# Optimization experiments

Measured on AMD Instinct MI355X. Metric: run time of the kernel, lower is better.

## Reference

```python
import jax, jax.numpy as jnp
import numpy as np

B, S, D, H, FF = 4, 2048, 512, 8, 2048
HD = D // H
SCALE = float(D) ** 0.5  # original scales by sqrt(embed_dim), not sqrt(head_dim)
EPS = 1e-5


def setup_inputs() -> dict:
    key = jax.random.key(0)
    ks = jax.random.split(key, 16)
    s_in = 1.0 / np.sqrt(D)
    s_ff = 1.0 / np.sqrt(FF)
    return {
        "embeddings": jax.random.normal(ks[0], (B, S, D), dtype=jnp.float32),
        "mask": jnp.ones((B, S), dtype=bool),
        # per-head Q/K/V projections stacked: [H, D, HD]
        "Wq": jax.random.uniform(ks[1], (H, D, HD), jnp.float32, -s_in, s_in),
        "bq": jax.random.uniform(ks[2], (H, HD), jnp.float32, -s_in, s_in),
        "Wk": jax.random.uniform(ks[3], (H, D, HD), jnp.float32, -s_in, s_in),
        "bk": jax.random.uniform(ks[4], (H, HD), jnp.float32, -s_in, s_in),
        "Wv": jax.random.uniform(ks[5], (H, D, HD), jnp.float32, -s_in, s_in),
        "bv": jax.random.uniform(ks[6], (H, HD), jnp.float32, -s_in, s_in),
        "Wc": jax.random.uniform(ks[7], (D, D), jnp.float32, -s_in, s_in),
        "bc": jax.random.uniform(ks[8], (D,), jnp.float32, -s_in, s_in),
        "W1": jax.random.uniform(ks[9], (D, FF), jnp.float32, -s_in, s_in),
        "b1": jax.random.uniform(ks[10], (FF,), jnp.float32, -s_in, s_in),
        "W2": jax.random.uniform(ks[11], (FF, D), jnp.float32, -s_ff, s_ff),
        "b2": jax.random.uniform(ks[12], (D,), jnp.float32, -s_ff, s_ff),
        "gamma": jnp.ones((D,), jnp.float32),
        "beta": jnp.zeros((D,), jnp.float32),
    }


def reference(embeddings, mask, Wq, bq, Wk, bk, Wv, bv, Wc, bc, W1, b1, W2, b2, gamma, beta):
    # Per-head projections batched into one einsum each: [B,H,S,HD]
    Q = jnp.einsum("bsd,hdf->bhsf", embeddings, Wq) + bq[:, None, :]
    K = jnp.einsum("bsd,hdf->bhsf", embeddings, Wk) + bk[:, None, :]
    V = jnp.einsum("bsd,hdf->bhsf", embeddings, Wv) + bv[:, None, :]
    # NOTE: the original computes a masked score tensor but then softmaxes the
    # UNMASKED scores (bug). We faithfully ignore the mask here.
    scores = jnp.einsum("bhsf,bhtf->bhst", Q, K) / SCALE  # [B,H,S,S]
    A = jax.nn.softmax(scores, axis=-1)
    Hh = jnp.einsum("bhst,bhtf->bhsf", A, V)  # [B,H,S,HD]
    # concat heads along feature dim (head h -> contiguous slice)
    Hcat = jnp.transpose(Hh, (0, 2, 1, 3)).reshape(B, S, D)
    Hp = Hcat @ Wc + bc
    # add & norm (dropout is identity at eval)
    res = Hp + embeddings
    mu = jnp.mean(res, axis=-1, keepdims=True)
    var = jnp.var(res, axis=-1, keepdims=True)
    Hn = (res - mu) / jnp.sqrt(var + EPS) * gamma + beta
    out = jax.nn.relu(Hn @ W1 + b1) @ W2 + b2  # no residual after FFN in original
    return out, mask
```

## Files before the change

### kernel.cpp

```cpp
#include <hip/hip_runtime.h>
#include <hip/hip_bf16.h>
#include <cstdint>
#include <cstddef>

typedef short  s16x8 __attribute__((ext_vector_type(8)));
typedef short  s16x4 __attribute__((ext_vector_type(4)));
typedef float  f32x4 __attribute__((ext_vector_type(4)));
typedef unsigned u32x2 __attribute__((ext_vector_type(2)));

static constexpr int Bb = 4, Ss = 2048, Dd = 512, Hh = 8, HDd = 64, FFf = 2048;
static constexpr int Mm = Bb * Ss;

__device__ __forceinline__ unsigned short f2bf(float f) {
  unsigned u = __float_as_uint(f);
  u += 0x7FFFu + ((u >> 16) & 1u);
  return (unsigned short)(u >> 16);
}

__device__ __forceinline__ unsigned cvt_pk_bf16(float lo, float hi) {
  unsigned r;
  asm("v_cvt_pk_bf16_f32 %0, %1, %2" : "=v"(r) : "v"(lo), "v"(hi));
  return r;
}

__device__ __forceinline__ float exp2_raw(float x) {
  float r;
  asm("v_exp_f32 %0, %1\n\ts_nop 0" : "=v"(r) : "v"(x));
  return r;
}

#define GLOAD_LDS16(gp, lp)                                                     \
  __builtin_amdgcn_global_load_lds((const __attribute__((address_space(1))) void*)(gp), \
                                   (__attribute__((address_space(3))) void*)(lp), 16, 0, 0)

__device__ __forceinline__ void xpose_tile(const float* __restrict__ in,
                                           unsigned short* __restrict__ out,
                                           int K, int N, int bx, int by, float (*t)[33]) {
  const int lx = threadIdx.x & 31, ly = threadIdx.x >> 5;
  const int n0 = bx * 32, k0 = by * 32;
#pragma unroll
  for (int r = 0; r < 4; ++r) t[ly + r * 8][lx] = in[(size_t)(k0 + ly + r * 8) * N + n0 + lx];
  __syncthreads();
#pragma unroll
  for (int r = 0; r < 4; ++r)
    out[(size_t)(n0 + ly + r * 8) * K + k0 + lx] = f2bf(t[lx][ly + r * 8]);
}

__global__ __launch_bounds__(256) void prep_all(
    const float* __restrict__ emb, const float* __restrict__ Wq, const float* __restrict__ Wk,
    const float* __restrict__ Wv, const float* __restrict__ Wc, const float* __restrict__ W1,
    const float* __restrict__ W2, unsigned short* __restrict__ embB,
    unsigned short* __restrict__ WtQKV, unsigned short* __restrict__ WtC,
    unsigned short* __restrict__ Wt1, unsigned short* __restrict__ Wt2,
    float* __restrict__ maskOut) {
  __shared__ float t[32][33];
  const int blk = blockIdx.x;
  if (blk < 4096) {
    const int i = blk * 256 + threadIdx.x;
    const float4 v = reinterpret_cast<const float4*>(emb)[i];
    s16x4 o; o[0] = f2bf(v.x); o[1] = f2bf(v.y); o[2] = f2bf(v.z); o[3] = f2bf(v.w);
    reinterpret_cast<s16x4*>(embB)[i] = o;
  } else if (blk < 4864) {
    const int b = blk - 4096;
    const int bx = b & 15, by = (b >> 4) & 1, z = b >> 5;
    const int sel = z >> 3, h = z & 7;
    const float* W = sel == 0 ? Wq : (sel == 1 ? Wk : Wv);
    const float* inb = W + (size_t)h * 512 * 64;
    unsigned short* outb = WtQKV + (size_t)sel * 512 * 512 + (size_t)h * 64 * 512;
    const int lx = threadIdx.x & 31, ly = threadIdx.x >> 5;
    const int d0 = bx * 32, f0 = by * 32;
#pragma unroll
    for (int r = 0; r < 4; ++r) t[ly + r * 8][lx] = inb[(size_t)(d0 + ly + r * 8) * 64 + f0 + lx];
    __syncthreads();
#pragma unroll
    for (int r = 0; r < 4; ++r)
      outb[(size_t)(f0 + ly + r * 8) * 512 + d0 + lx] = f2bf(t[lx][ly + r * 8]);
  } else if (blk < 5120) {
    const int b = blk - 4864;
    xpose_tile(Wc, WtC, 512, 512, b & 15, b >> 4, t);
  } else if (blk < 6144) {
    const int b = blk - 5120;
    xpose_tile(W1, Wt1, 512, 2048, b & 63, b >> 6, t);
  } else if (blk < 7168) {
    const int b = blk - 6144;
    xpose_tile(W2, Wt2, 2048, 512, b & 15, b >> 4, t);
  } else {
    const int i = (blk - 7168) * 256 + threadIdx.x;
    if (i < Bb * Ss) maskOut[i] = 1.0f;
  }
}

__global__ __launch_bounds__(256) void vtrans(const unsigned short* __restrict__ Vn,
                                              unsigned short* __restrict__ Vt) {
  __shared__ unsigned short t[64][72];
  const int bh = blockIdx.y, s0 = blockIdx.x * 64;
  const int row = threadIdx.x >> 2, cs = (threadIdx.x & 3) << 4;
  const unsigned short* src = Vn + (((size_t)bh * 2048 + s0 + row) << 6) + cs;
  *reinterpret_cast<s16x8*>(&t[row][cs]) = *reinterpret_cast<const s16x8*>(src);
  *reinterpret_cast<s16x8*>(&t[row][cs + 8]) = *reinterpret_cast<const s16x8*>(src + 8);
  __syncthreads();
  unsigned ow[8];
#pragma unroll
  for (int j = 0; j < 8; ++j)
    ow[j] = (unsigned)t[cs + 2 * j][row] | ((unsigned)t[cs + 2 * j + 1][row] << 16);
  unsigned short* dst = Vt + (((size_t)bh * 64 + row) << 11) + s0 + cs;
  *reinterpret_cast<uint4*>(dst) = *reinterpret_cast<const uint4*>(&ow[0]);
  *reinterpret_cast<uint4*>(dst + 8) = *reinterpret_cast<const uint4*>(&ow[4]);
}

template<int EPI, int NI>
__global__ __launch_bounds__(256) void gemm_bt(
    const unsigned short* __restrict__ A, const unsigned short* __restrict__ Bt,
    const float* __restrict__ bias0, const float* __restrict__ bias1, const float* __restrict__ bias2,
    const float* __restrict__ addf, float* __restrict__ outF,
    unsigned short* __restrict__ outB0, unsigned short* __restrict__ outB1,
    unsigned short* __restrict__ outB2, int M, int N, int K, int nbx) {
  constexpr int BN = NI * 32;
  __shared__ alignas(16) unsigned short As[3][128 * 32];
  __shared__ alignas(16) unsigned short Bs[3][BN * 32];
  const int tid = threadIdx.x;
  const int lane = tid & 63, wid = tid >> 6;
  const int wr = wid >> 1, wc = wid & 1;
  const int fr = lane & 15, kg = lane >> 4;

  const int lin = blockIdx.x;
  const int xcd = lin & 7, idx = lin >> 3;
  const int bx = idx % nbx, ysub = idx / nbx;
  const int m0 = (xcd * 8 + ysub) * 128, n0 = bx * BN;

  const int srow = tid >> 2;
  const int schunk = (tid & 3) ^ ((tid >> 3) & 3);
  const unsigned short* gA = A + (size_t)(m0 + srow) * K + (schunk << 3);
  const unsigned short* gB = Bt + (size_t)(n0 + srow) * K + (schunk << 3);

  auto STAGE = [&](int kt, int buf) {
    unsigned short* lA = &As[buf][wid * 512];
    unsigned short* lB = &Bs[buf][wid * 512];
    GLOAD_LDS16(gA + kt, lA);
    GLOAD_LDS16(gA + (size_t)64 * K + kt, lA + 2048);
    GLOAD_LDS16(gB + kt, lB);
    if constexpr (NI == 4) GLOAD_LDS16(gB + (size_t)64 * K + kt, lB + 2048);
  };

  f32x4 acc[4][NI];
#pragma unroll
  for (int i = 0; i < 4; ++i)
#pragma unroll
    for (int j = 0; j < NI; ++j)
#pragma unroll
      for (int r = 0; r < 4; ++r) acc[i][j][r] = 0.f;

  STAGE(0, 0);
  STAGE(32, 1);
  const int nk = K >> 5;
  int cur = 0;
  const int rchunk = (kg ^ ((fr >> 1) & 3)) << 3;
  for (int ki = 0; ki < nk; ++ki) {
    const int pre = cur == 0 ? 2 : cur - 1;
    __builtin_amdgcn_s_barrier();
    if (ki + 2 < nk) {
      STAGE((ki + 2) << 5, pre);
      if constexpr (NI == 4)
        asm volatile("s_waitcnt vmcnt(8)" ::: "memory");
      else
        asm volatile("s_waitcnt vmcnt(6)" ::: "memory");
    } else if (ki + 1 < nk) {
      if constexpr (NI == 4)
        asm volatile("s_waitcnt vmcnt(4)" ::: "memory");
      else
        asm volatile("s_waitcnt vmcnt(3)" ::: "memory");
    } else {
      asm volatile("s_waitcnt vmcnt(0)" ::: "memory");
    }
    __builtin_amdgcn_sched_barrier(0);
    __builtin_amdgcn_s_barrier();
    __builtin_amdgcn_sched_barrier(0);

    s16x8 af[4], bfv[NI];
#pragma unroll
    for (int i = 0; i < 4; ++i)
      af[i] = *reinterpret_cast<const s16x8*>(&As[cur][(wr * 64 + i * 16 + fr) * 32 + rchunk]);
#pragma unroll
    for (int i = 0; i < NI; ++i)
      bfv[i] = *reinterpret_cast<const s16x8*>(
          &Bs[cur][(wc * (NI * 16) + i * 16 + fr) * 32 + rchunk]);
    __builtin_amdgcn_s_setprio(1);
#pragma unroll
    for (int mi = 0; mi < 4; ++mi)
#pragma unroll
      for (int ni = 0; ni < NI; ++ni)
        acc[mi][ni] = __builtin_amdgcn_mfma_f32_16x16x32_bf16(af[mi], bfv[ni], acc[mi][ni], 0, 0, 0);
    __builtin_amdgcn_s_setprio(0);
    cur = cur == 2 ? 0 : cur + 1;
  }

#pragma unroll
  for (int mi = 0; mi < 4; ++mi)
#pragma unroll
    for (int ni = 0; ni < NI; ++ni)
#pragma unroll
      for (int r = 0; r < 4; ++r) {
        const int row = m0 + wr * 64 + mi * 16 + kg * 4 + r;
        const int col = n0 + wc * (NI * 16) + ni * 16 + fr;
        float v = acc[mi][ni][r];
        if constexpr (EPI == 0) {
          const int sel = col >> 9, c = col & 511;
          const float* bs = sel == 0 ? bias0 : (sel == 1 ? bias1 : bias2);
          v += bs[c];
          const int b = row >> 11, s = row & 2047;
          const int h = c >> 6, f = c & 63;
          unsigned short* ob = sel == 0 ? outB0 : (sel == 1 ? outB1 : outB2);
          ob[((size_t)((b << 3) + h) * 2048 + s) * 64 + f] = f2bf(v);
        } else if constexpr (EPI == 1) {
          const size_t idx2 = (size_t)row * 512 + col;
          outF[idx2] = v + bias0[col] + addf[idx2];
        } else if constexpr (EPI == 2) {
          v += bias0[col];
          outB0[(size_t)row * 2048 + col] = f2bf(v > 0.f ? v : 0.f);
        } else {
          outF[(size_t)row * 512 + col] = v + bias0[col];
        }
      }
}

__global__ __launch_bounds__(256) void attn_kernel(const unsigned short* __restrict__ Q,
                                                   const unsigned short* __restrict__ Kx,
                                                   const unsigned short* __restrict__ V,
                                                   unsigned short* __restrict__ Hcat) {
  const int lane = threadIdx.x & 63, wid = threadIdx.x >> 6;
  const int fr = lane & 15, kg = lane >> 4;
  const int lin = blockIdx.x;
  const int xcd = lin & 7, idx = lin >> 3;
  const int bh = xcd * 4 + (idx & 3);
  const int qi = idx >> 2;
  const int b = bh >> 3, h = bh & 7;
  const int q0 = qi * 64 + wid * 16;
  const unsigned short* Qh = Q + (size_t)bh * Ss * HDd;
  const unsigned short* Kh = Kx + (size_t)bh * Ss * HDd;
  const unsigned short* Vh = V + (size_t)bh * HDd * Ss;

  __shared__ alignas(16) unsigned short Ks[2][64 * 64];
  __shared__ alignas(16) unsigned short Vs[64 * 64];
  __shared__ alignas(16) unsigned short P[4][16][72];

  const int srow = lane >> 3;
  const int scol = ((lane & 7) ^ srow) << 3;
  const unsigned short* gK0 = Kh + (size_t)(8 * (2 * wid + 0) + srow) * 64 + scol;
  const unsigned short* gK1 = Kh + (size_t)(8 * (2 * wid + 1) + srow) * 64 + scol;
  const unsigned short* gV0 = Vh + (size_t)(8 * (2 * wid + 0) + srow) * 2048 + scol;
  const unsigned short* gV1 = Vh + (size_t)(8 * (2 * wid + 1) + srow) * 2048 + scol;
  unsigned short* lK0a = &Ks[0][(2 * wid + 0) * 512];
  unsigned short* lK1a = &Ks[0][(2 * wid + 1) * 512];
  unsigned short* lK0b = &Ks[1][(2 * wid + 0) * 512];
  unsigned short* lK1b = &Ks[1][(2 * wid + 1) * 512];
  unsigned short* lV0 = &Vs[(2 * wid + 0) * 512];
  unsigned short* lV1 = &Vs[(2 * wid + 1) * 512];

  s16x8 bq[2];
#pragma unroll
  for (int kb = 0; kb < 2; ++kb)
    bq[kb] = *reinterpret_cast<const s16x8*>(&Qh[(size_t)(q0 + fr) * 64 + kb * 32 + kg * 8]);

  f32x4 o[4];
#pragma unroll
  for (int ct = 0; ct < 4; ++ct)
#pragma unroll
    for (int r = 0; r < 4; ++r) o[ct][r] = 0.f;
  float mr = -1e30f, lsum = 0.f;

  const float iscL = 1.4426950408889634f * 0.044194173824159216f;
  const int swz = (fr & 7) << 3;

  GLOAD_LDS16(gK0, lK0a);
  GLOAD_LDS16(gK1, lK1a);
  GLOAD_LDS16(gV0, lV0);
  GLOAD_LDS16(gV1, lV1);

#pragma unroll 1
  for (int t = 0; t < 32; ++t) {
    const int kt = t * 64;
    const int ktn = (kt + 64) & 2047;
    const unsigned short* KsC = Ks[t & 1];
    unsigned short* nK0 = (t & 1) ? lK0a : lK0b;
    unsigned short* nK1 = (t & 1) ? lK1a : lK1b;

    asm volatile("s_waitcnt vmcnt(2)" ::: "memory");
    __builtin_amdgcn_sched_barrier(0);
    __builtin_amdgcn_s_barrier();
    __builtin_amdgcn_sched_barrier(0);

    f32x4 sc[4];
#pragma unroll
    for (int ct = 0; ct < 4; ++ct)
#pragma unroll
      for (int r = 0; r < 4; ++r) sc[ct][r] = 0.f;
    __builtin_amdgcn_s_setprio(1);
#pragma unroll
    for (int ct = 0; ct < 4; ++ct)
#pragma unroll
      for (int kb = 0; kb < 2; ++kb) {
        const s16x8 kf = *reinterpret_cast<const s16x8*>(
            &KsC[(ct * 16 + fr) * 64 + (((kg << 3) + (kb << 5)) ^ swz)]);
        sc[ct] = __builtin_amdgcn_mfma_f32_16x16x32_bf16(kf, bq[kb], sc[ct], 0, 0, 0);
      }
    __builtin_amdgcn_s_setprio(0);

    GLOAD_LDS16(gK0 + (size_t)ktn * 64, nK0);
    GLOAD_LDS16(gK1 + (size_t)ktn * 64, nK1);

    float mxl;
    {
      const float a0 = fmaxf(fmaxf(sc[0][0], sc[0][1]), fmaxf(sc[0][2], sc[0][3]));
      const float a1 = fmaxf(fmaxf(sc[1][0], sc[1][1]), fmaxf(sc[1][2], sc[1][3]));
      const float a2 = fmaxf(fmaxf(sc[2][0], sc[2][1]), fmaxf(sc[2][2], sc[2][3]));
      const float a3 = fmaxf(fmaxf(sc[3][0], sc[3][1]), fmaxf(sc[3][2], sc[3][3]));
      mxl = fmaxf(fmaxf(a0, a1), fmaxf(a2, a3)) * iscL;
    }
    if (!__all(mxl <= mr + 8.0f)) {
      float mx = fmaxf(mxl, __shfl_xor(mxl, 16));
      mx = fmaxf(mx, __shfl_xor(mx, 32));
      const float mn = fmaxf(mr, mx);
      const float corr = exp2_raw(mr - mn);
      mr = mn;
      lsum *= corr;
      float corrq[4];
#pragma unroll
      for (int r = 0; r < 4; ++r) corrq[r] = __shfl(corr, kg * 4 + r);
#pragma unroll
      for (int ct = 0; ct < 4; ++ct)
#pragma unroll
        for (int r = 0; r < 4; ++r) o[ct][r] *= corrq[r];
    }

    float ps0 = 0.f, ps1 = 0.f;
#pragma unroll
    for (int ct = 0; ct < 4; ++ct) {
      float p0 = exp2_raw(__builtin_fmaf(sc[ct][0], iscL, -mr));
      float p1 = exp2_raw(__builtin_fmaf(sc[ct][1], iscL, -mr));
      float p2 = exp2_raw(__builtin_fmaf(sc[ct][2], iscL, -mr));
      float p3 = exp2_raw(__builtin_fmaf(sc[ct][3], iscL, -mr));
      ps0 += (p0 + p1);
      ps1 += (p2 + p3);
      u32x2 pk;
      pk[0] = cvt_pk_bf16(p0, p1);
      pk[1] = cvt_pk_bf16(p2, p3);
      *reinterpret_cast<u32x2*>(&P[wid][fr][ct * 16 + kg * 4]) = pk;
    }
    lsum += ps0 + ps1;

    asm volatile("s_waitcnt vmcnt(2)" ::: "memory");
    __builtin_amdgcn_sched_barrier(0);
    __builtin_amdgcn_s_barrier();
    __builtin_amdgcn_sched_barrier(0);

    const s16x8 pa0 = *reinterpret_cast<const s16x8*>(&P[wid][fr][kg * 8]);
    const s16x8 pa1 = *reinterpret_cast<const s16x8*>(&P[wid][fr][32 + kg * 8]);
    __builtin_amdgcn_s_setprio(1);
#pragma unroll
    for (int ct = 0; ct < 4; ++ct) {
      const s16x8 bv0 = *reinterpret_cast<const s16x8*>(
          &Vs[(ct * 16 + fr) * 64 + (((kg << 3) + 0) ^ swz)]);
      o[ct] = __builtin_amdgcn_mfma_f32_16x16x32_bf16(pa0, bv0, o[ct], 0, 0, 0);
      const s16x8 bv1 = *reinterpret_cast<const s16x8*>(
          &Vs[(ct * 16 + fr) * 64 + (((kg << 3) + 32) ^ swz)]);
      o[ct] = __builtin_amdgcn_mfma_f32_16x16x32_bf16(pa1, bv1, o[ct], 0, 0, 0);
    }
    __builtin_amdgcn_s_setprio(0);

    __builtin_amdgcn_s_barrier();
    __builtin_amdgcn_sched_barrier(0);
    GLOAD_LDS16(gV0 + ktn, lV0);
    GLOAD_LDS16(gV1 + ktn, lV1);
  }

  lsum += __shfl_xor(lsum, 16);
  lsum += __shfl_xor(lsum, 32);
  float invq[4];
#pragma unroll
  for (int r = 0; r < 4; ++r) invq[r] = 1.0f / __shfl(lsum, kg * 4 + r);
#pragma unroll
  for (int ct = 0; ct < 4; ++ct)
#pragma unroll
    for (int r = 0; r < 4; ++r) {
      const int qrow = q0 + kg * 4 + r;
      Hcat[(size_t)(b * Ss + qrow) * Dd + h * 64 + ct * 16 + fr] = f2bf(o[ct][r] * invq[r]);
    }
}

__global__ __launch_bounds__(256) void layernorm_k(const float* __restrict__ res,
                                                   const float* __restrict__ gamma,
                                                   const float* __restrict__ beta,
                                                   unsigned short* __restrict__ out) {
  const int lane = threadIdx.x & 63, wid = threadIdx.x >> 6;
  const int row = blockIdx.x * 4 + wid;
  const float* rp = res + (size_t)row * 512 + lane * 8;
  const float4 v0 = *reinterpret_cast<const float4*>(rp);
  const float4 v1 = *reinterpret_cast<const float4*>(rp + 4);
  float x[8] = {v0.x, v0.y, v0.z, v0.w, v1.x, v1.y, v1.z, v1.w};
  float s = 0.f, q = 0.f;
#pragma unroll
  for (int j = 0; j < 8; ++j) { s += x[j]; q += x[j] * x[j]; }
#pragma unroll
  for (int off = 32; off; off >>= 1) { s += __shfl_xor(s, off); q += __shfl_xor(q, off); }
  const float mean = s * (1.f / 512.f);
  const float var = q * (1.f / 512.f) - mean * mean;
  const float rstd = rsqrtf(var + 1e-5f);
  s16x8 o;
#pragma unroll
  for (int j = 0; j < 8; ++j) {
    const int c = lane * 8 + j;
    o[j] = f2bf((x[j] - mean) * rstd * gamma[c] + beta[c]);
  }
  *reinterpret_cast<s16x8*>(out + (size_t)row * 512 + lane * 8) = o;
}

extern "C" void kernel_launch(void* const* d_in, const int* in_sizes, int n_in,
                              void* d_out, int out_size, void* d_ws, size_t ws_size,
                              hipStream_t stream) {
  const float* emb = (const float*)d_in[0];
  const float* Wq = (const float*)d_in[2];
  const float* bq = (const float*)d_in[3];
  const float* Wk = (const float*)d_in[4];
  const float* bk = (const float*)d_in[5];
  const float* Wv = (const float*)d_in[6];
  const float* bv = (const float*)d_in[7];
  const float* Wc = (const float*)d_in[8];
  const float* bc = (const float*)d_in[9];
  const float* W1 = (const float*)d_in[10];
  const float* b1 = (const float*)d_in[11];
  const float* W2 = (const float*)d_in[12];
  const float* b2 = (const float*)d_in[13];
  const float* gamma = (const float*)d_in[14];
  const float* beta = (const float*)d_in[15];
  float* out = (float*)d_out;

  char* ws = (char*)d_ws;
  size_t off = 0;
  auto alloc = [&](size_t bytes) {
    char* p = ws + off;
    off = (off + bytes + 255) & ~(size_t)255;
    return p;
  };
  unsigned short* embB = (unsigned short*)alloc((size_t)Mm * Dd * 2);
  unsigned short* WtQKV = (unsigned short*)alloc((size_t)1536 * 512 * 2);
  unsigned short* WtC = (unsigned short*)alloc((size_t)512 * 512 * 2);
  unsigned short* Wt1 = (unsigned short*)alloc((size_t)2048 * 512 * 2);
  unsigned short* Wt2 = (unsigned short*)alloc((size_t)512 * 2048 * 2);
  unsigned short* Qb = (unsigned short*)alloc((size_t)Mm * Dd * 2);
  unsigned short* Kb = (unsigned short*)alloc((size_t)Mm * Dd * 2);
  unsigned short* Vt = (unsigned short*)alloc((size_t)Mm * Dd * 2);
  unsigned short* Hcat = (unsigned short*)alloc((size_t)Mm * Dd * 2);
  float* resF = (float*)alloc((size_t)Mm * Dd * 4);
  unsigned short* HnB = (unsigned short*)alloc((size_t)Mm * Dd * 2);
  unsigned short* G = Qb;
  unsigned short* Vn = HnB;

  prep_all<<<7200, 256, 0, stream>>>(emb, Wq, Wk, Wv, Wc, W1, W2,
                                     embB, WtQKV, WtC, Wt1, Wt2,
                                     out + (size_t)Mm * Dd);

  gemm_bt<0, 4><<<768, 256, 0, stream>>>(embB, WtQKV, bq, bk, bv, nullptr, nullptr,
                                         Qb, Kb, Vn, Mm, 1536, 512, 12);
  vtrans<<<dim3(32, 32), 256, 0, stream>>>(Vn, Vt);
  attn_kernel<<<1024, 256, 0, stream>>>(Qb, Kb, Vt, Hcat);
  gemm_bt<1, 2><<<512, 256, 0, stream>>>(Hcat, WtC, bc, nullptr, nullptr, emb, resF,
                                         nullptr, nullptr, nullptr, Mm, 512, 512, 8);
  layernorm_k<<<2048, 256, 0, stream>>>(resF, gamma, beta, HnB);
  gemm_bt<2, 4><<<1024, 256, 0, stream>>>(HnB, Wt1, b1, nullptr, nullptr, nullptr, nullptr,
                                          G, nullptr, nullptr, Mm, 2048, 512, 16);
  gemm_bt<3, 2><<<512, 256, 0, stream>>>(G, Wt2, b2, nullptr, nullptr, nullptr, out,
                                         nullptr, nullptr, nullptr, Mm, 512, 2048, 8);
}
```

Measured before the change: 177.5 us.

## Fuse V transpose into QKV GEMM epilogue and double attention block size

The QKV projection epilogue now writes V directly in transposed [bh, f, s] layout using packed 4-element stores, which removes the separate vtrans kernel launch and its extra read and write of V. The attention kernel moves to 512-thread blocks covering 128 query rows. Each wave now issues one K and one V tile load instead of two, and half as many blocks each reuse a K/V tile across twice as many queries. The larger blocks may lower occupancy and add barrier cost across eight waves.

```diff
diff --git a/kernel.cpp b/kernel.cpp
--- a/kernel.cpp
+++ b/kernel.cpp
@@ -90,24 +90,6 @@
   }
 }
 
-__global__ __launch_bounds__(256) void vtrans(const unsigned short* __restrict__ Vn,
-                                              unsigned short* __restrict__ Vt) {
-  __shared__ unsigned short t[64][72];
-  const int bh = blockIdx.y, s0 = blockIdx.x * 64;
-  const int row = threadIdx.x >> 2, cs = (threadIdx.x & 3) << 4;
-  const unsigned short* src = Vn + (((size_t)bh * 2048 + s0 + row) << 6) + cs;
-  *reinterpret_cast<s16x8*>(&t[row][cs]) = *reinterpret_cast<const s16x8*>(src);
-  *reinterpret_cast<s16x8*>(&t[row][cs + 8]) = *reinterpret_cast<const s16x8*>(src + 8);
-  __syncthreads();
-  unsigned ow[8];
-#pragma unroll
-  for (int j = 0; j < 8; ++j)
-    ow[j] = (unsigned)t[cs + 2 * j][row] | ((unsigned)t[cs + 2 * j + 1][row] << 16);
-  unsigned short* dst = Vt + (((size_t)bh * 64 + row) << 11) + s0 + cs;
-  *reinterpret_cast<uint4*>(dst) = *reinterpret_cast<const uint4*>(&ow[0]);
-  *reinterpret_cast<uint4*>(dst + 8) = *reinterpret_cast<const uint4*>(&ow[4]);
-}
-
 template<int EPI, int NI>
 __global__ __launch_bounds__(256) void gemm_bt(
     const unsigned short* __restrict__ A, const unsigned short* __restrict__ Bt,
@@ -197,33 +179,52 @@
 #pragma unroll
   for (int mi = 0; mi < 4; ++mi)
 #pragma unroll
-    for (int ni = 0; ni < NI; ++ni)
-#pragma unroll
-      for (int r = 0; r < 4; ++r) {
-        const int row = m0 + wr * 64 + mi * 16 + kg * 4 + r;
+    for (int ni = 0; ni < NI; ++ni) {
+      if constexpr (EPI == 0) {
         const int col = n0 + wc * (NI * 16) + ni * 16 + fr;
-        float v = acc[mi][ni][r];
-        if constexpr (EPI == 0) {
-          const int sel = col >> 9, c = col & 511;
-          const float* bs = sel == 0 ? bias0 : (sel == 1 ? bias1 : bias2);
-          v += bs[c];
-          const int b = row >> 11, s = row & 2047;
-          const int h = c >> 6, f = c & 63;
-          unsigned short* ob = sel == 0 ? outB0 : (sel == 1 ? outB1 : outB2);
-          ob[((size_t)((b << 3) + h) * 2048 + s) * 64 + f] = f2bf(v);
-        } else if constexpr (EPI == 1) {
-          const size_t idx2 = (size_t)row * 512 + col;
-          outF[idx2] = v + bias0[col] + addf[idx2];
-        } else if constexpr (EPI == 2) {
-          v += bias0[col];
-          outB0[(size_t)row * 2048 + col] = f2bf(v > 0.f ? v : 0.f);
+        const int sel = col >> 9, c = col & 511;
+        const int h = c >> 6, f = c & 63;
+        const int row0 = m0 + wr * 64 + mi * 16 + kg * 4;
+        const int b = row0 >> 11, s0 = row0 & 2047;
+        if (sel == 2) {
+          const float bsv = bias2[c];
+          u32x2 pk;
+          pk[0] = (unsigned)f2bf(acc[mi][ni][0] + bsv) |
+                  ((unsigned)f2bf(acc[mi][ni][1] + bsv) << 16);
+          pk[1] = (unsigned)f2bf(acc[mi][ni][2] + bsv) |
+                  ((unsigned)f2bf(acc[mi][ni][3] + bsv) << 16);
+          *reinterpret_cast<u32x2*>(
+              &outB2[((size_t)((b << 3) + h) * 64 + f) * 2048 + s0]) = pk;
         } else {
-          outF[(size_t)row * 512 + col] = v + bias0[col];
+          const float* bs = sel == 0 ? bias0 : bias1;
+          unsigned short* ob = sel == 0 ? outB0 : outB1;
+          const float bv = bs[c];
+#pragma unroll
+          for (int r = 0; r < 4; ++r)
+            ob[((size_t)((b << 3) + h) * 2048 + s0 + r) * 64 + f] =
+                f2bf(acc[mi][ni][r] + bv);
+        }
+      } else {
+#pragma unroll
+        for (int r = 0; r < 4; ++r) {
+          const int row = m0 + wr * 64 + mi * 16 + kg * 4 + r;
+          const int col = n0 + wc * (NI * 16) + ni * 16 + fr;
+          float v = acc[mi][ni][r];
+          if constexpr (EPI == 1) {
+            const size_t idx2 = (size_t)row * 512 + col;
+            outF[idx2] = v + bias0[col] + addf[idx2];
+          } else if constexpr (EPI == 2) {
+            v += bias0[col];
+            outB0[(size_t)row * 2048 + col] = f2bf(v > 0.f ? v : 0.f);
+          } else {
+            outF[(size_t)row * 512 + col] = v + bias0[col];
+          }
         }
       }
-}
-
-__global__ __launch_bounds__(256) void attn_kernel(const unsigned short* __restrict__ Q,
+    }
+}
+
+__global__ __launch_bounds__(512) void attn_kernel(const unsigned short* __restrict__ Q,
                                                    const unsigned short* __restrict__ Kx,
                                                    const unsigned short* __restrict__ V,
                                                    unsigned short* __restrict__ Hcat) {
@@ -234,27 +235,22 @@
   const int bh = xcd * 4 + (idx & 3);
   const int qi = idx >> 2;
   const int b = bh >> 3, h = bh & 7;
-  const int q0 = qi * 64 + wid * 16;
+  const int q0 = qi * 128 + wid * 16;
   const unsigned short* Qh = Q + (size_t)bh * Ss * HDd;
   const unsigned short* Kh = Kx + (size_t)bh * Ss * HDd;
   const unsigned short* Vh = V + (size_t)bh * HDd * Ss;
 
   __shared__ alignas(16) unsigned short Ks[2][64 * 64];
   __shared__ alignas(16) unsigned short Vs[64 * 64];
-  __shared__ alignas(16) unsigned short P[4][16][72];
+  __shared__ alignas(16) unsigned short P[8][16][72];
 
   const int srow = lane >> 3;
   const int scol = ((lane & 7) ^ srow) << 3;
-  const unsigned short* gK0 = Kh + (size_t)(8 * (2 * wid + 0) + srow) * 64 + scol;
-  const unsigned short* gK1 = Kh + (size_t)(8 * (2 * wid + 1) + srow) * 64 + scol;
-  const unsigned short* gV0 = Vh + (size_t)(8 * (2 * wid + 0) + srow) * 2048 + scol;
-  const unsigned short* gV1 = Vh + (size_t)(8 * (2 * wid + 1) + srow) * 2048 + scol;
-  unsigned short* lK0a = &Ks[0][(2 * wid + 0) * 512];
-  unsigned short* lK1a = &Ks[0][(2 * wid + 1) * 512];
-  unsigned short* lK0b = &Ks[1][(2 * wid + 0) * 512];
-  unsigned short* lK1b = &Ks[1][(2 * wid + 1) * 512];
-  unsigned short* lV0 = &Vs[(2 * wid + 0) * 512];
-  unsigned short* lV1 = &Vs[(2 * wid + 1) * 512];
+  const unsigned short* gK = Kh + (size_t)(8 * wid + srow) * 64 + scol;
+  const unsigned short* gV = Vh + (size_t)(8 * wid + srow) * 2048 + scol;
+  unsigned short* lKa = &Ks[0][wid * 512];
+  unsigned short* lKb = &Ks[1][wid * 512];
+  unsigned short* lV  = &Vs[wid * 512];
 
   s16x8 bq[2];
 #pragma unroll
@@ -271,20 +267,17 @@
   const float iscL = 1.4426950408889634f * 0.044194173824159216f;
   const int swz = (fr & 7) << 3;
 
-  GLOAD_LDS16(gK0, lK0a);
-  GLOAD_LDS16(gK1, lK1a);
-  GLOAD_LDS16(gV0, lV0);
-  GLOAD_LDS16(gV1, lV1);
+  GLOAD_LDS16(gK, lKa);
+  GLOAD_LDS16(gV, lV);
 
 #pragma unroll 1
   for (int t = 0; t < 32; ++t) {
     const int kt = t * 64;
     const int ktn = (kt + 64) & 2047;
     const unsigned short* KsC = Ks[t & 1];
-    unsigned short* nK0 = (t & 1) ? lK0a : lK0b;
-    unsigned short* nK1 = (t & 1) ? lK1a : lK1b;
-
-    asm volatile("s_waitcnt vmcnt(2)" ::: "memory");
+    unsigned short* nK = (t & 1) ? lKa : lKb;
+
+    asm volatile("s_waitcnt vmcnt(1)" ::: "memory");
     __builtin_amdgcn_sched_barrier(0);
     __builtin_amdgcn_s_barrier();
     __builtin_amdgcn_sched_barrier(0);
@@ -305,8 +298,7 @@
       }
     __builtin_amdgcn_s_setprio(0);
 
-    GLOAD_LDS16(gK0 + (size_t)ktn * 64, nK0);
-    GLOAD_LDS16(gK1 + (size_t)ktn * 64, nK1);
+    GLOAD_LDS16(gK + (size_t)ktn * 64, nK);
 
     float mxl;
     {
@@ -348,7 +340,7 @@
     }
     lsum += ps0 + ps1;
 
-    asm volatile("s_waitcnt vmcnt(2)" ::: "memory");
+    asm volatile("s_waitcnt vmcnt(1)" ::: "memory");
     __builtin_amdgcn_sched_barrier(0);
     __builtin_amdgcn_s_barrier();
     __builtin_amdgcn_sched_barrier(0);
@@ -369,8 +361,7 @@
 
     __builtin_amdgcn_s_barrier();
     __builtin_amdgcn_sched_barrier(0);
-    GLOAD_LDS16(gV0 + ktn, lV0);
-    GLOAD_LDS16(gV1 + ktn, lV1);
+    GLOAD_LDS16(gV + ktn, lV);
   }
 
   lsum += __shfl_xor(lsum, 16);
@@ -453,16 +444,14 @@
   float* resF = (float*)alloc((size_t)Mm * Dd * 4);
   unsigned short* HnB = (unsigned short*)alloc((size_t)Mm * Dd * 2);
   unsigned short* G = Qb;
-  unsigned short* Vn = HnB;
 
   prep_all<<<7200, 256, 0, stream>>>(emb, Wq, Wk, Wv, Wc, W1, W2,
                                      embB, WtQKV, WtC, Wt1, Wt2,
                                      out + (size_t)Mm * Dd);
 
   gemm_bt<0, 4><<<768, 256, 0, stream>>>(embB, WtQKV, bq, bk, bv, nullptr, nullptr,
-                                         Qb, Kb, Vn, Mm, 1536, 512, 12);
-  vtrans<<<dim3(32, 32), 256, 0, stream>>>(Vn, Vt);
-  attn_kernel<<<1024, 256, 0, stream>>>(Qb, Kb, Vt, Hcat);
+                                         Qb, Kb, Vt, Mm, 1536, 512, 12);
+  attn_kernel<<<512, 512, 0, stream>>>(Qb, Kb, Vt, Hcat);
   gemm_bt<1, 2><<<512, 256, 0, stream>>>(Hcat, WtC, bc, nullptr, nullptr, emb, resF,
                                          nullptr, nullptr, nullptr, Mm, 512, 512, 8);
   layernorm_k<<<2048, 256, 0, stream>>>(resF, gamma, beta, HnB);
```

Result: faster. 166.3 us (-6.3%).
